# Optimization experiments

Hardware: AMD Instinct MI355X
Metric: run time of the kernel (lower is better)

The kernel has to match this reference:

```python
import jax, jax.numpy as jnp
import numpy as np

B, P, N, D = 128, 2048, 256, 2

def setup_inputs() -> dict:
    key = jax.random.key(0)
    k1, k2, k3 = jax.random.split(key, 3)
    batch = jax.random.normal(k1, (B, P, D), dtype=jnp.float32)
    not_dummy = jnp.ones((B, P), dtype=jnp.float32)
    centers = jax.random.uniform(k2, (N, D), dtype=jnp.float32)
    sharpness = jax.random.uniform(k3, (N, D), dtype=jnp.float32)
    exponent = jnp.ones((1,), dtype=jnp.float32)
    return {"batch": batch, "not_dummy": not_dummy, "centers": centers,
            "sharpness": sharpness, "exponent": exponent}

def reference(batch, not_dummy, centers, sharpness, exponent):
    # batch: (B, P, D); centers/sharpness: (N, D); exponent: (1,)
    # weighted L1 distance from each point to each structure element: (B, N, P)
    diff = jnp.abs(centers[None, :, None, :] - batch[:, None, :, :])
    s = jnp.sum(diff * jnp.abs(sharpness)[None, :, None, :], axis=-1)
    # rational kernel, mask out dummy (padding) points, sum-pool over points
    r = 1.0 / (1.0 + s ** exponent[0])
    r = r * not_dummy[:, None, :]
    return jnp.sum(r, axis=-1)  # (B, N)
```

## Files before the change

kernel.cpp:

```cpp
#include <hip/hip_runtime.h>

constexpr int B   = 128;
constexpr int P   = 2048;
constexpr int N   = 256;
constexpr int TPB = 256;
constexpr int CPW = 8;
constexpr int NPB = 32;
constexpr int HV  = 16;

__device__ __forceinline__ float rdfl(float v) {
    return __int_as_float(__builtin_amdgcn_readfirstlane(__float_as_int(v)));
}

__global__ __launch_bounds__(TPB, 4)
void SLayerRational_43190191128606_kernel(
    const float* __restrict__ batch,
    const float* __restrict__ not_dummy,
    const float* __restrict__ centers,
    const float* __restrict__ sharpness,
    const float* __restrict__ exponent,
    float* __restrict__ out)
{
    const int b    = blockIdx.x >> 3;
    const int n0   = (blockIdx.x & 7) * NPB;
    const int wave = threadIdx.x >> 6;
    const int lane = threadIdx.x & 63;
    const int nw   = n0 + wave * CPW;

    float c0[CPW], c1[CPW], a0[CPW], a1[CPW];
#pragma unroll
    for (int c = 0; c < CPW; ++c) {
        c0[c] = rdfl(centers[(nw + c) * 2 + 0]);
        c1[c] = rdfl(centers[(nw + c) * 2 + 1]);
        a0[c] = rdfl(fabsf(sharpness[(nw + c) * 2 + 0]));
        a1[c] = rdfl(fabsf(sharpness[(nw + c) * 2 + 1]));
    }
    const float e = exponent[0];

    float acc[CPW];
#pragma unroll
    for (int c = 0; c < CPW; ++c) acc[c] = 0.0f;

    if (e == 1.0f) {
        const float4* bb4 = reinterpret_cast<const float4*>(batch) + (size_t)b * (P / 2);
        const float2* nd2 = reinterpret_cast<const float2*>(not_dummy) + (size_t)b * (P / 2);

        float4 xq[HV];
        float2 wq[HV];
#pragma unroll
        for (int k = 0; k < HV; ++k) {
            xq[k] = bb4[k * 64 + lane];
            wq[k] = nd2[k * 64 + lane];
        }

#pragma unroll
        for (int c = 0; c < CPW; ++c) {
#pragma unroll
            for (int k = 0; k < HV; ++k) {
                const float4 x = xq[k];
                const float2 w = wq[k];
                const float ua = fmaf(fabsf(c0[c] - x.x), a0[c],
                                  fmaf(fabsf(c1[c] - x.y), a1[c], 1.0f));
                acc[c] = fmaf(w.x, __builtin_amdgcn_rcpf(ua), acc[c]);
                const float ub = fmaf(fabsf(c0[c] - x.z), a0[c],
                                  fmaf(fabsf(c1[c] - x.w), a1[c], 1.0f));
                acc[c] = fmaf(w.y, __builtin_amdgcn_rcpf(ub), acc[c]);
            }
        }
    } else {
        const float2* bb = reinterpret_cast<const float2*>(batch) + (size_t)b * P;
        const float*  nd = not_dummy + (size_t)b * P;
        for (int it = 0; it < P / 64; ++it) {
            const int p = it * 64 + lane;
            const float2 x = bb[p];
            const float  w = nd[p];
#pragma unroll
            for (int c = 0; c < CPW; ++c) {
                const float s = fmaf(fabsf(c0[c] - x.x), a0[c],
                                     fabsf(c1[c] - x.y) * a1[c]);
                acc[c] += w / (1.0f + powf(s, e));
            }
        }
    }

#pragma unroll
    for (int c = 0; c < CPW; ++c) {
#pragma unroll
        for (int off = 32; off > 0; off >>= 1)
            acc[c] += __shfl_down(acc[c], off, 64);
    }

    if (lane == 0) {
#pragma unroll
        for (int c = 0; c < CPW; ++c)
            out[b * N + nw + c] = acc[c];
    }
}

extern "C" void kernel_launch(void* const* d_in, const int* in_sizes, int n_in,
                              void* d_out, int out_size, void* d_ws, size_t ws_size,
                              hipStream_t stream) {
    const float* batch     = (const float*)d_in[0];
    const float* not_dummy = (const float*)d_in[1];
    const float* centers   = (const float*)d_in[2];
    const float* sharpness = (const float*)d_in[3];
    const float* exponent  = (const float*)d_in[4];
    float* out = (float*)d_out;

    const int blocks = B * (N / NPB);
    SLayerRational_43190191128606_kernel<<<blocks, TPB, 0, stream>>>(
        batch, not_dummy, centers, sharpness, exponent, out);
}
```

Before: 19.47 us.

## Split points across waves, pair reciprocals, and use halved xor-shuffle reduction

Each block now handles 8 centers instead of 32, and its four waves split the 2048 points among themselves rather than splitting centers. This cuts per-thread register arrays and raises the occupancy hint from 4 to 8 blocks per CU. The inner loop merges two rcp calls into one by computing (w.x*ub + w.y*ua)/(ua*ub). The wave reduction packs two accumulators per shuffle, then a shared-memory step sums the four waves' partials. The trade-off is a block sync and LDS traffic, plus more blocks that each reload centers. The product of denominators also carries some extra rounding risk.

```diff
diff --git a/kernel.cpp b/kernel.cpp
--- a/kernel.cpp
+++ b/kernel.cpp
@@ -4,15 +4,14 @@
 constexpr int P   = 2048;
 constexpr int N   = 256;
 constexpr int TPB = 256;
-constexpr int CPW = 8;
-constexpr int NPB = 32;
-constexpr int HV  = 16;
+constexpr int NPB = 8;
+constexpr int KQ  = 4;
 
 __device__ __forceinline__ float rdfl(float v) {
     return __int_as_float(__builtin_amdgcn_readfirstlane(__float_as_int(v)));
 }
 
-__global__ __launch_bounds__(TPB, 4)
+__global__ __launch_bounds__(TPB, 8)
 void SLayerRational_43190191128606_kernel(
     const float* __restrict__ batch,
     const float* __restrict__ not_dummy,
@@ -21,61 +20,65 @@
     const float* __restrict__ exponent,
     float* __restrict__ out)
 {
-    const int b    = blockIdx.x >> 3;
-    const int n0   = (blockIdx.x & 7) * NPB;
+    const int b    = blockIdx.x >> 5;
+    const int n0   = (blockIdx.x & 31) * NPB;
     const int wave = threadIdx.x >> 6;
     const int lane = threadIdx.x & 63;
-    const int nw   = n0 + wave * CPW;
 
-    float c0[CPW], c1[CPW], a0[CPW], a1[CPW];
+    float c0[NPB], c1[NPB], a0[NPB], a1[NPB];
 #pragma unroll
-    for (int c = 0; c < CPW; ++c) {
-        c0[c] = rdfl(centers[(nw + c) * 2 + 0]);
-        c1[c] = rdfl(centers[(nw + c) * 2 + 1]);
-        a0[c] = rdfl(fabsf(sharpness[(nw + c) * 2 + 0]));
-        a1[c] = rdfl(fabsf(sharpness[(nw + c) * 2 + 1]));
+    for (int c = 0; c < NPB; ++c) {
+        c0[c] = rdfl(centers[(n0 + c) * 2 + 0]);
+        c1[c] = rdfl(centers[(n0 + c) * 2 + 1]);
+        a0[c] = rdfl(fabsf(sharpness[(n0 + c) * 2 + 0]));
+        a1[c] = rdfl(fabsf(sharpness[(n0 + c) * 2 + 1]));
     }
     const float e = exponent[0];
 
-    float acc[CPW];
+    float acc[NPB];
 #pragma unroll
-    for (int c = 0; c < CPW; ++c) acc[c] = 0.0f;
+    for (int c = 0; c < NPB; ++c) acc[c] = 0.0f;
 
     if (e == 1.0f) {
-        const float4* bb4 = reinterpret_cast<const float4*>(batch) + (size_t)b * (P / 2);
-        const float2* nd2 = reinterpret_cast<const float2*>(not_dummy) + (size_t)b * (P / 2);
+        const float4* bb4 = reinterpret_cast<const float4*>(batch)
+                          + (size_t)b * (P / 2) + wave * 256;
+        const float2* nd2 = reinterpret_cast<const float2*>(not_dummy)
+                          + (size_t)b * (P / 2) + wave * 256;
 
-        float4 xq[HV];
-        float2 wq[HV];
+        float4 xq[KQ];
+        float2 wq[KQ];
 #pragma unroll
-        for (int k = 0; k < HV; ++k) {
+        for (int k = 0; k < KQ; ++k) {
             xq[k] = bb4[k * 64 + lane];
             wq[k] = nd2[k * 64 + lane];
         }
 
 #pragma unroll
-        for (int c = 0; c < CPW; ++c) {
+        for (int c = 0; c < NPB; ++c) {
 #pragma unroll
-            for (int k = 0; k < HV; ++k) {
+            for (int k = 0; k < KQ; ++k) {
                 const float4 x = xq[k];
                 const float2 w = wq[k];
                 const float ua = fmaf(fabsf(c0[c] - x.x), a0[c],
                                   fmaf(fabsf(c1[c] - x.y), a1[c], 1.0f));
-                acc[c] = fmaf(w.x, __builtin_amdgcn_rcpf(ua), acc[c]);
                 const float ub = fmaf(fabsf(c0[c] - x.z), a0[c],
                                   fmaf(fabsf(c1[c] - x.w), a1[c], 1.0f));
-                acc[c] = fmaf(w.y, __builtin_amdgcn_rcpf(ub), acc[c]);
+                float num = w.x * ub;
+                num = fmaf(w.y, ua, num);
+                const float den = ua * ub;
+                acc[c] = fmaf(num, __builtin_amdgcn_rcpf(den), acc[c]);
             }
         }
     } else {
-        const float2* bb = reinterpret_cast<const float2*>(batch) + (size_t)b * P;
-        const float*  nd = not_dummy + (size_t)b * P;
-        for (int it = 0; it < P / 64; ++it) {
+        const float2* bb = reinterpret_cast<const float2*>(batch)
+                         + (size_t)b * P + wave * 512;
+        const float*  nd = not_dummy + (size_t)b * P + wave * 512;
+        for (int it = 0; it < 8; ++it) {
             const int p = it * 64 + lane;
             const float2 x = bb[p];
             const float  w = nd[p];
 #pragma unroll
-            for (int c = 0; c < CPW; ++c) {
+            for (int c = 0; c < NPB; ++c) {
                 const float s = fmaf(fabsf(c0[c] - x.x), a0[c],
                                      fabsf(c1[c] - x.y) * a1[c]);
                 acc[c] += w / (1.0f + powf(s, e));
@@ -83,17 +86,31 @@
         }
     }
 
+    const bool lo = (lane < 32);
+    float r[4];
 #pragma unroll
-    for (int c = 0; c < CPW; ++c) {
+    for (int j = 0; j < 4; ++j) {
+        const float m = lo ? acc[j] : acc[j + 4];
+        const float o = lo ? acc[j + 4] : acc[j];
+        r[j] = m + __shfl_xor(o, 32, 64);
+    }
 #pragma unroll
-        for (int off = 32; off > 0; off >>= 1)
-            acc[c] += __shfl_down(acc[c], off, 64);
+    for (int j = 0; j < 4; ++j) {
+#pragma unroll
+        for (int off = 16; off > 0; off >>= 1)
+            r[j] += __shfl_xor(r[j], off, 64);
     }
 
-    if (lane == 0) {
-#pragma unroll
-        for (int c = 0; c < CPW; ++c)
-            out[b * N + nw + c] = acc[c];
+    __shared__ float red[4][NPB];
+    if ((lane & 31) == 0) {
+        float4* dst = reinterpret_cast<float4*>(&red[wave][(lane >> 5) * 4]);
+        *dst = make_float4(r[0], r[1], r[2], r[3]);
+    }
+    __syncthreads();
+
+    if (threadIdx.x < NPB) {
+        const int t = threadIdx.x;
+        out[b * N + n0 + t] = red[0][t] + red[1][t] + red[2][t] + red[3][t];
     }
 }
 
```

New measurement: 20.30 us. 1.04x slower.
